# Kernel tuning notes

Measured on AMD Instinct MI355X. Metric: run time of the kernel, lower is better.

## Reference

```python
import jax, jax.numpy as jnp
import numpy as np

SIZE = (128.0, 128.0, 128.0)
FEATURE_BLOCK_IDS = (1, 2, 3)


def _trilerp(feat, coords, power):
    # feat: [B, D, H, W, C]; coords: [B, N, 3] in [0, 1]
    B = coords.shape[0]
    scale = jnp.asarray([0.5 ** power * SIZE[0],
                         0.5 ** power * SIZE[1],
                         0.5 ** power * SIZE[2]], dtype=coords.dtype)
    hi = float(min(feat.shape[1:4])) - 1.01
    idx = jnp.clip(coords * scale, 0.01, hi)  # [B, N, 3]
    ix, iy, iz = idx[..., 0], idx[..., 1], idx[..., 2]
    x1, x2 = jnp.floor(ix), jnp.ceil(ix)
    y1, y2 = jnp.floor(iy), jnp.ceil(iy)
    z1, z2 = jnp.floor(iz), jnp.ceil(iz)
    b = jnp.arange(B)[:, None]  # broadcast batch index

    def g(xi, yi, zi):
        return feat[b, xi.astype(jnp.int32), yi.astype(jnp.int32), zi.astype(jnp.int32)]

    wx, wx2 = (ix - x1)[..., None], (x2 - ix)[..., None]
    wy, wy2 = (iy - y1)[..., None], (y2 - iy)[..., None]
    wz, wz2 = (iz - z1)[..., None], (z2 - iz)[..., None]

    # z = z1 plane
    lerp_x1 = g(x2, y1, z1) * wx + g(x1, y1, z1) * wx2
    lerp_x2 = g(x2, y2, z1) * wx + g(x1, y2, z1) * wx2
    lerp_y1 = lerp_x2 * wy + lerp_x1 * wy2
    # z = z2 plane
    lerp_x1 = g(x2, y1, z2) * wx + g(x1, y1, z2) * wx2
    lerp_x2 = g(x2, y2, z2) * wx + g(x1, y2, z2) * wx2
    lerp_y2 = lerp_x2 * wy + lerp_x1 * wy2
    return lerp_y2 * wz + lerp_y1 * wz2  # [B, N, C]


def setup_inputs() -> dict:
    key = jax.random.key(0)
    ks = jax.random.split(key, 7)
    B, N = 2, 50000
    return {
        'features0': jax.random.normal(ks[0], (B, 128, 128, 128, 1), jnp.float32),
        'features1': jax.random.normal(ks[1], (B, 64, 64, 64, 32), jnp.float32),
        'features2': jax.random.normal(ks[2], (B, 32, 32, 32, 64), jnp.float32),
        'features3': jax.random.normal(ks[3], (B, 16, 16, 16, 128), jnp.float32),
        'features4': jax.random.normal(ks[4], (B, 8, 8, 8, 256), jnp.float32),
        'mesh_coords': jax.random.uniform(ks[5], (B, N, 3), jnp.float32),
        'mesh_features': jax.random.normal(ks[6], (B, N, 3), jnp.float32),
    }


def reference(features0, features1, features2, features3, features4, mesh_coords, mesh_features):
    feats = [features0, features1, features2, features3, features4]
    # mesh_coords is [B, N, 3] -> one coord group, reshape is identity
    sampled = [_trilerp(feats[i], mesh_coords, i) for i in FEATURE_BLOCK_IDS]
    out = jnp.concatenate(sampled, axis=-1)
    return jnp.concatenate([out, mesh_features], axis=-1)
```

## Files before the change

### kernel.cpp

```cpp
#include <hip/hip_runtime.h>


typedef float floatx4 __attribute__((ext_vector_type(4)));

__device__ __forceinline__ int point_batch(int p, int N) {
    int b = 0;
    while (p >= N) { p -= N; ++b; }
    return b;
}

__device__ __forceinline__ int bucket_of(const float* __restrict__ coords,
                                         int p, int N) {
    const float cx = coords[p * 3 + 0];
    const float cy = coords[p * 3 + 1];
    const float cz = coords[p * 3 + 2];
    int bx = (int)(cx * 16.0f); bx = bx < 0 ? 0 : (bx > 15 ? 15 : bx);
    int by = (int)(cy * 16.0f); by = by < 0 ? 0 : (by > 15 ? 15 : by);
    int bz = (int)(cz * 16.0f); bz = bz < 0 ? 0 : (bz > 15 ? 15 : bz);
    return ((point_batch(p, N) * 16 + bx) * 16 + by) * 16 + bz;
}

__global__ __launch_bounds__(256) void hist_kernel(
    const float* __restrict__ coords, unsigned* __restrict__ bins,
    int N, int P)
{
    const int p = blockIdx.x * 256 + (int)threadIdx.x;
    if (p < P) atomicAdd(&bins[bucket_of(coords, p, N)], 1u);
}

__global__ __launch_bounds__(1024) void scan_kernel(unsigned* __restrict__ bins)
{
    __shared__ unsigned part[1024];
    const int t = threadIdx.x;
    unsigned loc[8];
    unsigned s = 0;
    for (int i = 0; i < 8; ++i) {
        unsigned v = bins[t * 8 + i];
        loc[i] = s;
        s += v;
    }
    part[t] = s;
    __syncthreads();
    for (int off = 1; off < 1024; off <<= 1) {
        unsigned v = (t >= off) ? part[t - off] : 0u;
        __syncthreads();
        part[t] += v;
        __syncthreads();
    }
    const unsigned base = (t == 0) ? 0u : part[t - 1];
    for (int i = 0; i < 8; ++i) bins[t * 8 + i] = base + loc[i];
}

__global__ __launch_bounds__(256) void scatter_kernel(
    const float* __restrict__ coords, unsigned* __restrict__ bins,
    unsigned* __restrict__ perm, float* __restrict__ csort,
    int N, int P)
{
    const int p = blockIdx.x * 256 + (int)threadIdx.x;
    if (p < P) {
        const unsigned pos = atomicAdd(&bins[bucket_of(coords, p, N)], 1u);
        perm[pos] = (unsigned)p;
        csort[pos * 3 + 0] = coords[p * 3 + 0];
        csort[pos * 3 + 1] = coords[p * 3 + 1];
        csort[pos * 3 + 2] = coords[p * 3 + 2];
    }
}

__device__ __forceinline__ int seg_swz(int lo, int S) {
    const int q = S >> 3, r = S & 7;
    const int xcd = lo & 7, j = lo >> 3;
    return (xcd < r ? xcd * (q + 1) : r * (q + 1) + (xcd - r) * q) + j;
}

template<int D, int LPP, int OCB>
__device__ __forceinline__ void do_level(const float* __restrict__ fbase,
                                         const float* __restrict__ coords,
                                         const float* __restrict__ csort,
                                         const unsigned* __restrict__ perm,
                                         float* __restrict__ out,
                                         int sBase, int N, int P)
{
    const int tid  = threadIdx.x;
    const int lane = tid & 63;
    const int wv   = tid >> 6;
    const int slot = sBase + wv * (64 / LPP) + (lane / LPP);
    const int c4   = lane & (LPP - 1);
    if (slot >= P) return;
    const int p = perm ? (int)perm[slot] : slot;

    const float* cp = csort ? (csort + slot * 3) : (coords + p * 3);
    const float cx = cp[0];
    const float cy = cp[1];
    const float cz = cp[2];

    const float scale = (float)D;
    const float hi    = (float)((double)D - 1.01);

    const float ix = fminf(fmaxf(cx * scale, 0.01f), hi);
    const float iy = fminf(fmaxf(cy * scale, 0.01f), hi);
    const float iz = fminf(fmaxf(cz * scale, 0.01f), hi);

    const float x1f = floorf(ix), x2f = ceilf(ix);
    const float y1f = floorf(iy), y2f = ceilf(iy);
    const float z1f = floorf(iz), z2f = ceilf(iz);
    const int x1 = (int)x1f, x2 = (int)x2f;
    const int y1 = (int)y1f, y2 = (int)y2f;
    const int z1 = (int)z1f, z2 = (int)z2f;

    const float wx = ix - x1f, wx2 = x2f - ix;
    const float wy = iy - y1f, wy2 = y2f - iy;
    const float wz = iz - z1f, wz2 = z2f - iz;

    const unsigned baseB = (unsigned)point_batch(p, N) * (unsigned)(D * D * D * LPP * 16)
                         + (unsigned)c4 * 16u;
    #define OFFB(X, Y, Z) (baseB + (unsigned)((((X) * D + (Y)) * D + (Z)) * LPP) * 16u)

    floatx4 v111, v211, v121, v221, v112, v212, v122, v222;
    asm volatile("global_load_dwordx4 %0, %1, %2"
                 : "=v"(v111) : "v"(OFFB(x1, y1, z1)), "s"(fbase));
    asm volatile("global_load_dwordx4 %0, %1, %2"
                 : "=v"(v211) : "v"(OFFB(x2, y1, z1)), "s"(fbase));
    asm volatile("global_load_dwordx4 %0, %1, %2"
                 : "=v"(v121) : "v"(OFFB(x1, y2, z1)), "s"(fbase));
    asm volatile("global_load_dwordx4 %0, %1, %2"
                 : "=v"(v221) : "v"(OFFB(x2, y2, z1)), "s"(fbase));
    asm volatile("global_load_dwordx4 %0, %1, %2"
                 : "=v"(v112) : "v"(OFFB(x1, y1, z2)), "s"(fbase));
    asm volatile("global_load_dwordx4 %0, %1, %2"
                 : "=v"(v212) : "v"(OFFB(x2, y1, z2)), "s"(fbase));
    asm volatile("global_load_dwordx4 %0, %1, %2"
                 : "=v"(v122) : "v"(OFFB(x1, y2, z2)), "s"(fbase));
    asm volatile("global_load_dwordx4 %0, %1, %2"
                 : "=v"(v222) : "v"(OFFB(x2, y2, z2)), "s"(fbase));
    #undef OFFB

    asm volatile("s_waitcnt vmcnt(0)");
    __builtin_amdgcn_sched_barrier(0);

    const floatx4 lx1a = v211 * wx + v111 * wx2;
    const floatx4 lx2a = v221 * wx + v121 * wx2;
    const floatx4 ly1  = lx2a * wy + lx1a * wy2;
    const floatx4 lx1b = v212 * wx + v112 * wx2;
    const floatx4 lx2b = v222 * wx + v122 * wx2;
    const floatx4 ly2  = lx2b * wy + lx1b * wy2;
    const floatx4 r    = ly2  * wz + ly1  * wz2;

    float* o = out + p * 227 + OCB + c4 * 4;
    __builtin_nontemporal_store(r.x, o + 0);
    __builtin_nontemporal_store(r.y, o + 1);
    __builtin_nontemporal_store(r.z, o + 2);
    __builtin_nontemporal_store(r.w, o + 3);
}

__global__ __launch_bounds__(256, 8) void trilerp_kernel(
    const float* __restrict__ f1,
    const float* __restrict__ f2,
    const float* __restrict__ f3,
    const float* __restrict__ coords,
    const float* __restrict__ meshf,
    const float* __restrict__ csort,
    const unsigned* __restrict__ perm,
    float* __restrict__ out,
    int N, int P, int nb1, int nb2, int nb3)
{
    const int orig = (int)blockIdx.x;
    if (orig < nb1) {
        const int blk = seg_swz(orig, nb1);
        do_level<64, 8, 0>(f1, coords, csort, perm, out, blk * 32, N, P);
    } else if (orig < nb1 + nb2) {
        const int blk = seg_swz(orig - nb1, nb2);
        do_level<32, 16, 32>(f2, coords, csort, perm, out, blk * 16, N, P);
    } else if (orig < nb1 + nb2 + nb3) {
        const int blk = seg_swz(orig - nb1 - nb2, nb3);
        do_level<16, 32, 96>(f3, coords, csort, perm, out, blk * 8, N, P);
    } else {
        const int e = (orig - nb1 - nb2 - nb3) * 256 + (int)threadIdx.x;
        if (e < P * 3) {
            const int p = e / 3, c = e - p * 3;
            __builtin_nontemporal_store(meshf[e], &out[p * 227 + 224 + c]);
        }
    }
}

extern "C" void kernel_launch(void* const* d_in, const int* in_sizes, int n_in,
                              void* d_out, int out_size, void* d_ws, size_t ws_size,
                              hipStream_t stream) {
    const float* f1     = (const float*)d_in[1];
    const float* f2     = (const float*)d_in[2];
    const float* f3     = (const float*)d_in[3];
    const float* coords = (const float*)d_in[5];
    const float* meshf  = (const float*)d_in[6];
    float* out = (float*)d_out;

    const int B = in_sizes[1] / (64 * 64 * 64 * 32);
    const int N = in_sizes[5] / (B * 3);
    const int P = B * N;

    const int NBINS = 8192;
    const size_t ws_need = (size_t)NBINS * 4 + (size_t)P * 4 + (size_t)P * 12;
    unsigned* bins  = (unsigned*)d_ws;
    unsigned* perm  = bins + NBINS;
    float*    csort = (float*)(perm + P);
    const bool do_sort = (d_ws != nullptr) && (ws_size >= ws_need);

    if (do_sort) {
        hipMemsetAsync(bins, 0, NBINS * 4, stream);
        const int nbp = (P + 255) / 256;
        hist_kernel<<<dim3(nbp), dim3(256), 0, stream>>>(coords, bins, N, P);
        scan_kernel<<<dim3(1), dim3(1024), 0, stream>>>(bins);
        scatter_kernel<<<dim3(nbp), dim3(256), 0, stream>>>(coords, bins, perm,
                                                            csort, N, P);
    }

    const int nb1 = (P + 31) / 32;
    const int nb2 = (P + 15) / 16;
    const int nb3 = (P + 7) / 8;
    const int nbm = (P * 3 + 255) / 256;
    const int grid = nb1 + nb2 + nb3 + nbm;

    trilerp_kernel<<<dim3(grid), dim3(256), 0, stream>>>(
        f1, f2, f3, coords, meshf,
        do_sort ? csort : nullptr, do_sort ? perm : nullptr,
        out, N, P, nb1, nb2, nb3);
}
```

Baseline: 232.8 us.

## Stage per-bucket feature tiles in LDS for levels 2 and 3

```diff
diff --git a/kernel.cpp b/kernel.cpp
--- a/kernel.cpp
+++ b/kernel.cpp
@@ -2,6 +2,8 @@
 
 
 typedef float floatx4 __attribute__((ext_vector_type(4)));
+
+#define NBINS 8192
 
 __device__ __forceinline__ int point_batch(int p, int N) {
     int b = 0;
@@ -72,6 +74,103 @@
     return (xcd < r ? xcd * (q + 1) : r * (q + 1) + (xcd - r) * q) + j;
 }
 
+template<int D, int C, int OCB, int NC>
+__device__ __forceinline__ void do_bucket(const float* __restrict__ fbase,
+                                          const unsigned* __restrict__ bins,
+                                          const float* __restrict__ csort,
+                                          const unsigned* __restrict__ perm,
+                                          float* __restrict__ out,
+                                          int bid, float* __restrict__ lds)
+{
+    constexpr int LPP = C / 4;
+    constexpr int SB  = D / 16;
+    const int tid = threadIdx.x;
+
+    const int s = (bid ? (int)bins[bid - 1] : 0);
+    const int e = (int)bins[bid];
+    if (s >= e) return;
+
+    const int b  = bid >> 12;
+    const int bx = (bid >> 8) & 15;
+    const int by = (bid >> 4) & 15;
+    const int bz = bid & 15;
+    const int xt = min(bx * SB, D - NC);
+    const int yt = min(by * SB, D - NC);
+    const int zt = min(bz * SB, D - NC);
+
+    constexpr int CHPC   = C / 4;
+    constexpr int CHUNKS = NC * NC * NC * CHPC;
+    for (int t = tid; t < CHUNKS; t += 256) {
+        const int cell = t / CHPC;
+        const int w    = t & (CHPC - 1);
+        const int dx = cell / (NC * NC);
+        const int rem = cell - dx * NC * NC;
+        const int dy = rem / NC;
+        const int dz = rem - dy * NC;
+        const int gx = xt + dx, gy = yt + dy, gz = zt + dz;
+        const int goff = (((b * D + gx) * D + gy) * D + gz) * C + w * 4;
+        *(floatx4*)(lds + cell * C + w * 4) = *(const floatx4*)(fbase + goff);
+    }
+    __syncthreads();
+
+    constexpr int PPP = 256 / LPP;
+    const int lp = tid / LPP;
+    const int c4 = tid & (LPP - 1);
+    const floatx4* T = (const floatx4*)lds;
+
+    const float scale = (float)D;
+    const float hi    = (float)((double)D - 1.01);
+
+    for (int base = s; base < e; base += PPP) {
+        const int slot = base + lp;
+        if (slot >= e) continue;
+
+        const float cx = csort[slot * 3 + 0];
+        const float cy = csort[slot * 3 + 1];
+        const float cz = csort[slot * 3 + 2];
+
+        const float ix = fminf(fmaxf(cx * scale, 0.01f), hi);
+        const float iy = fminf(fmaxf(cy * scale, 0.01f), hi);
+        const float iz = fminf(fmaxf(cz * scale, 0.01f), hi);
+
+        const float x1f = floorf(ix), x2f = ceilf(ix);
+        const float y1f = floorf(iy), y2f = ceilf(iy);
+        const float z1f = floorf(iz), z2f = ceilf(iz);
+        const int lx1 = (int)x1f - xt, lx2 = (int)x2f - xt;
+        const int ly1 = (int)y1f - yt, ly2 = (int)y2f - yt;
+        const int lz1 = (int)z1f - zt, lz2 = (int)z2f - zt;
+
+        const float wx = ix - x1f, wx2 = x2f - ix;
+        const float wy = iy - y1f, wy2 = y2f - iy;
+        const float wz = iz - z1f, wz2 = z2f - iz;
+
+        #define LT(LX, LY, LZ) T[((((LX) * NC + (LY)) * NC + (LZ)) * LPP) + c4]
+        const floatx4 v111 = LT(lx1, ly1, lz1);
+        const floatx4 v211 = LT(lx2, ly1, lz1);
+        const floatx4 v121 = LT(lx1, ly2, lz1);
+        const floatx4 v221 = LT(lx2, ly2, lz1);
+        const floatx4 v112 = LT(lx1, ly1, lz2);
+        const floatx4 v212 = LT(lx2, ly1, lz2);
+        const floatx4 v122 = LT(lx1, ly2, lz2);
+        const floatx4 v222 = LT(lx2, ly2, lz2);
+        #undef LT
+
+        const floatx4 lx1a = v211 * wx + v111 * wx2;
+        const floatx4 lx2a = v221 * wx + v121 * wx2;
+        const floatx4 ly1v = lx2a * wy + lx1a * wy2;
+        const floatx4 lx1b = v212 * wx + v112 * wx2;
+        const floatx4 lx2b = v222 * wx + v122 * wx2;
+        const floatx4 ly2v = lx2b * wy + lx1b * wy2;
+        const floatx4 r    = ly2v * wz + ly1v * wz2;
+
+        float* o = out + (int)perm[slot] * 227 + OCB + c4 * 4;
+        __builtin_nontemporal_store(r.x, o + 0);
+        __builtin_nontemporal_store(r.y, o + 1);
+        __builtin_nontemporal_store(r.z, o + 2);
+        __builtin_nontemporal_store(r.w, o + 3);
+    }
+}
+
 template<int D, int LPP, int OCB>
 __device__ __forceinline__ void do_level(const float* __restrict__ fbase,
                                          const float* __restrict__ coords,
@@ -160,19 +259,44 @@
     const float* __restrict__ meshf,
     const float* __restrict__ csort,
     const unsigned* __restrict__ perm,
+    const unsigned* __restrict__ bins,
     float* __restrict__ out,
+    int N, int P, int nb1)
+{
+    __shared__ float tile[3 * 3 * 3 * 64];
+    const int orig = (int)blockIdx.x;
+
+    if (orig < NBINS) {
+        const int bid = seg_swz(orig, NBINS);
+        do_bucket<16, 128, 96, 2>(f3, bins, csort, perm, out, bid, tile);
+    } else if (orig < 2 * NBINS) {
+        const int bid = seg_swz(orig - NBINS, NBINS);
+        do_bucket<32, 64, 32, 3>(f2, bins, csort, perm, out, bid, tile);
+    } else if (orig < 2 * NBINS + nb1) {
+        const int blk = seg_swz(orig - 2 * NBINS, nb1);
+        do_level<64, 8, 0>(f1, coords, csort, perm, out, blk * 32, N, P);
+    } else {
+        const int e = (orig - 2 * NBINS - nb1) * 256 + (int)threadIdx.x;
+        if (e < P * 3) {
+            const int p = e / 3, c = e - p * 3;
+            __builtin_nontemporal_store(meshf[e], &out[p * 227 + 224 + c]);
+        }
+    }
+}
+
+__global__ __launch_bounds__(256, 8) void trilerp_fallback_kernel(
+    const float* __restrict__ f1, const float* __restrict__ f2,
+    const float* __restrict__ f3, const float* __restrict__ coords,
+    const float* __restrict__ meshf, float* __restrict__ out,
     int N, int P, int nb1, int nb2, int nb3)
 {
     const int orig = (int)blockIdx.x;
     if (orig < nb1) {
-        const int blk = seg_swz(orig, nb1);
-        do_level<64, 8, 0>(f1, coords, csort, perm, out, blk * 32, N, P);
+        do_level<64, 8, 0>(f1, coords, nullptr, nullptr, out, orig * 32, N, P);
     } else if (orig < nb1 + nb2) {
-        const int blk = seg_swz(orig - nb1, nb2);
-        do_level<32, 16, 32>(f2, coords, csort, perm, out, blk * 16, N, P);
+        do_level<32, 16, 32>(f2, coords, nullptr, nullptr, out, (orig - nb1) * 16, N, P);
     } else if (orig < nb1 + nb2 + nb3) {
-        const int blk = seg_swz(orig - nb1 - nb2, nb3);
-        do_level<16, 32, 96>(f3, coords, csort, perm, out, blk * 8, N, P);
+        do_level<16, 32, 96>(f3, coords, nullptr, nullptr, out, (orig - nb1 - nb2) * 8, N, P);
     } else {
         const int e = (orig - nb1 - nb2 - nb3) * 256 + (int)threadIdx.x;
         if (e < P * 3) {
@@ -196,12 +320,14 @@
     const int N = in_sizes[5] / (B * 3);
     const int P = B * N;
 
-    const int NBINS = 8192;
     const size_t ws_need = (size_t)NBINS * 4 + (size_t)P * 4 + (size_t)P * 12;
     unsigned* bins  = (unsigned*)d_ws;
     unsigned* perm  = bins + NBINS;
     float*    csort = (float*)(perm + P);
     const bool do_sort = (d_ws != nullptr) && (ws_size >= ws_need);
+
+    const int nb1 = (P + 31) / 32;
+    const int nbm = (P * 3 + 255) / 256;
 
     if (do_sort) {
         hipMemsetAsync(bins, 0, NBINS * 4, stream);
@@ -210,16 +336,14 @@
         scan_kernel<<<dim3(1), dim3(1024), 0, stream>>>(bins);
         scatter_kernel<<<dim3(nbp), dim3(256), 0, stream>>>(coords, bins, perm,
                                                             csort, N, P);
-    }
-
-    const int nb1 = (P + 31) / 32;
-    const int nb2 = (P + 15) / 16;
-    const int nb3 = (P + 7) / 8;
-    const int nbm = (P * 3 + 255) / 256;
-    const int grid = nb1 + nb2 + nb3 + nbm;
-
-    trilerp_kernel<<<dim3(grid), dim3(256), 0, stream>>>(
-        f1, f2, f3, coords, meshf,
-        do_sort ? csort : nullptr, do_sort ? perm : nullptr,
-        out, N, P, nb1, nb2, nb3);
-}
+        const int grid = 2 * NBINS + nb1 + nbm;
+        trilerp_kernel<<<dim3(grid), dim3(256), 0, stream>>>(
+            f1, f2, f3, coords, meshf, csort, perm, bins, out, N, P, nb1);
+    } else {
+        const int nb2 = (P + 15) / 16;
+        const int nb3 = (P + 7) / 8;
+        const int grid = nb1 + nb2 + nb3 + nbm;
+        trilerp_fallback_kernel<<<dim3(grid), dim3(256), 0, stream>>>(
+            f1, f2, f3, coords, meshf, out, N, P, nb1, nb2, nb3);
+    }
+}
```

New measurement: 228.7 us. Within noise of the previous version (-1.8%).
